# Kernel optimization log

Hardware: AMD Instinct MI355X
Metric: run time of the kernel (lower is better)

Reference implementation:

```python
import jax, jax.numpy as jnp
import numpy as np

BETA = 0.9
THRESHOLD = 1.0

B, T, I, H, O = 64, 512, 256, 512, 256


def setup_inputs() -> dict:
    key = jax.random.key(0)
    ks = jax.random.split(key, 10)
    s_in = 1.0 / np.sqrt(I)
    s_h = 1.0 / np.sqrt(H)
    return {
        "x": jax.random.normal(ks[0], (B, T, I), dtype=jnp.float32),
        "W_in": jax.random.uniform(ks[1], (H, I), jnp.float32, -s_in, s_in),
        "b_in": jax.random.uniform(ks[2], (H,), jnp.float32, -s_in, s_in),
        "W_ih": jax.random.uniform(ks[3], (H, H), jnp.float32, -s_h, s_h),
        "b_ih": jax.random.uniform(ks[4], (H,), jnp.float32, -s_h, s_h),
        "W_hh": jax.random.uniform(ks[5], (H, H), jnp.float32, -s_h, s_h),
        "b_hh": jax.random.uniform(ks[6], (H,), jnp.float32, -s_h, s_h),
        "W_out": jax.random.uniform(ks[7], (O, H), jnp.float32, -s_h, s_h),
        "b_out": jax.random.uniform(ks[8], (O,), jnp.float32, -s_h, s_h),
        "temporal_attention": jax.random.normal(ks[9], (T, O), dtype=jnp.float32),
    }


def _lif(mem, cur):
    # LIF with 'subtract' reset: new_mem*(1-s) + s*(new_mem-thr) == new_mem - s*thr
    new_mem = BETA * mem + cur
    spike = (new_mem > THRESHOLD).astype(new_mem.dtype)
    return new_mem - spike * THRESHOLD, spike


def reference(x, W_in, b_in, W_ih, b_ih, W_hh, b_hh, W_out, b_out, temporal_attention):
    dtype = x.dtype
    batch, time_steps, _ = x.shape
    hidden = W_in.shape[0]

    # Input projection for all time steps at once: (B,T,H) -> scan over T.
    input_proj = jnp.einsum('bti,hi->tbh', x, W_in) + b_in  # (T,B,H)

    mem0 = jnp.zeros((batch, hidden), dtype=dtype)
    _, hidden_spikes = jax.lax.scan(_lif, mem0, input_proj)  # (T,B,H)

    # Recurrent layer: input->hidden projection precomputed; hidden->hidden uses
    # carried membrane potential (as in the torch module).
    in_proj = jnp.einsum('tbh,gh->tbg', hidden_spikes, W_ih) + b_ih  # (T,B,H)

    def rec_step(mem, ip):
        total = ip + mem @ W_hh.T + b_hh
        return _lif(mem, total)

    _, temporal_spikes = jax.lax.scan(rec_step, mem0, in_proj)  # (T,B,H)

    out_proj = jnp.einsum('tbh,oh->tbo', temporal_spikes, W_out) + b_out  # (T,B,O)

    attn = jax.nn.softmax(temporal_attention[:time_steps], axis=0)  # (T,O)
    attended = jnp.einsum('tbo,to->bo', out_proj, attn)  # (B,O)

    # Final LIF from zero membrane: new_mem = attended; spike = (attended > thr)
    final_spikes = (attended > THRESHOLD).astype(dtype)
    return final_spikes
```

## Files before the change

### kernel.cpp

```cpp
#include <hip/hip_runtime.h>
#include <hip/hip_bf16.h>
#include <cstdint>


#define T_STEPS 512
#define BATCH 64
#define HID 512
#define IN_DIM 256
#define OUT_DIM 256
#define BETA 0.9f
#define THR 1.0f
#define SENT 0x7FC00000u

typedef __attribute__((ext_vector_type(8))) short short8;
typedef __attribute__((ext_vector_type(4))) float float4v;
typedef unsigned short ushort_t;

__global__ __launch_bounds__(256) void k_fill_nan(uint32_t* __restrict__ P) {
  const int idx = blockIdx.x * 256 + threadIdx.x;
  uint4 s = make_uint4(SENT, SENT, SENT, SENT);
  uint4* p4 = (uint4*)P;
  for (int i = idx; i < (32768 * 512) / 4; i += 65536) p4[i] = s;
}

__global__ __launch_bounds__(256) void k_split(const float* __restrict__ src,
                                               ushort_t* __restrict__ hi,
                                               ushort_t* __restrict__ lo, int n) {
  int i = blockIdx.x * 256 + threadIdx.x;
  const int stride = gridDim.x * 256;
  for (; i < n; i += stride) {
    float v = src[i];
    uint32_t u = __float_as_uint(v);
    uint32_t rh = u + 0x7FFFu + ((u >> 16) & 1u);
    ushort_t h = (ushort_t)(rh >> 16);
    float hf = __uint_as_float(((uint32_t)h) << 16);
    float l = v - hf;
    uint32_t ul = __float_as_uint(l);
    uint32_t rl = ul + 0x7FFFu + ((ul >> 16) & 1u);
    hi[i] = h;
    lo[i] = (ushort_t)(rl >> 16);
  }
}

__global__ __launch_bounds__(256) void k_softmax_t(
    const float* __restrict__ TA, float* __restrict__ attn) {
  __shared__ float redm[8][32];
  __shared__ float reds[8][32];
  const int ol = threadIdx.x & 31;
  const int tg = threadIdx.x >> 5;
  const int o = blockIdx.x * 32 + ol;
  float mx = -1e30f;
  for (int i = 0; i < 64; ++i) {
    float v = TA[(size_t)(tg * 64 + i) * OUT_DIM + o];
    mx = fmaxf(mx, v);
  }
  redm[tg][ol] = mx;
  __syncthreads();
  float m = redm[0][ol];
#pragma unroll
  for (int j = 1; j < 8; ++j) m = fmaxf(m, redm[j][ol]);
  float s = 0.f;
  for (int i = 0; i < 64; ++i) {
    float v = TA[(size_t)(tg * 64 + i) * OUT_DIM + o];
    s += __expf(v - m);
  }
  reds[tg][ol] = s;
  __syncthreads();
  float tot = 0.f;
#pragma unroll
  for (int j = 0; j < 8; ++j) tot += reds[j][ol];
  const float inv = 1.0f / tot;
  for (int i = 0; i < 64; ++i) {
    int t = tg * 64 + i;
    float v = TA[(size_t)t * OUT_DIM + o];
    attn[(size_t)t * OUT_DIM + o] = __expf(v - m) * inv;
  }
}

__global__ __launch_bounds__(256) void k_gemm_split3(
    const ushort_t* __restrict__ Ahi, const ushort_t* __restrict__ Alo,
    const ushort_t* __restrict__ Bhi, const ushort_t* __restrict__ Blo,
    const float* __restrict__ bias, float* __restrict__ C,
    int M, int N, int K) {
  __shared__ ushort_t At[2][128 * 40];
  __shared__ ushort_t Bt[2][128 * 40];
  const int tid = threadIdx.x;
  const int row0 = blockIdx.x * 128, col0 = blockIdx.y * 128;
  const int w = tid >> 6, lane = tid & 63;
  const int wm = (w >> 1) * 64, wn = (w & 1) * 64;
  const int l15 = lane & 15, quad = lane >> 4;
  float4v acc[4][4];
#pragma unroll
  for (int i = 0; i < 4; ++i)
#pragma unroll
    for (int j = 0; j < 4; ++j) acc[i][j] = (float4v){0.f, 0.f, 0.f, 0.f};

  for (int k0 = 0; k0 < K; k0 += 32) {
#pragma unroll
    for (int it = 0; it < 2; ++it) {
      int idx = it * 256 + tid;
      int r = idx >> 2;
      int c8 = (idx & 3) << 3;
      *(uint4*)(&At[0][r * 40 + c8]) =
          *(const uint4*)(&Ahi[(size_t)(row0 + r) * K + k0 + c8]);
      *(uint4*)(&At[1][r * 40 + c8]) =
          *(const uint4*)(&Alo[(size_t)(row0 + r) * K + k0 + c8]);
      *(uint4*)(&Bt[0][r * 40 + c8]) =
          *(const uint4*)(&Bhi[(size_t)(col0 + r) * K + k0 + c8]);
      *(uint4*)(&Bt[1][r * 40 + c8]) =
          *(const uint4*)(&Blo[(size_t)(col0 + r) * K + k0 + c8]);
    }
    __syncthreads();
    short8 ah[4], al[4], bh[4], bl[4];
    const int koff = quad * 8;
#pragma unroll
    for (int i = 0; i < 4; ++i) {
      ah[i] = *(const short8*)(&At[0][(wm + i * 16 + l15) * 40 + koff]);
      al[i] = *(const short8*)(&At[1][(wm + i * 16 + l15) * 40 + koff]);
      bh[i] = *(const short8*)(&Bt[0][(wn + i * 16 + l15) * 40 + koff]);
      bl[i] = *(const short8*)(&Bt[1][(wn + i * 16 + l15) * 40 + koff]);
    }
#pragma unroll
    for (int i = 0; i < 4; ++i)
#pragma unroll
      for (int j = 0; j < 4; ++j) {
        acc[i][j] = __builtin_amdgcn_mfma_f32_16x16x32_bf16(ah[i], bh[j], acc[i][j], 0, 0, 0);
        acc[i][j] = __builtin_amdgcn_mfma_f32_16x16x32_bf16(ah[i], bl[j], acc[i][j], 0, 0, 0);
        acc[i][j] = __builtin_amdgcn_mfma_f32_16x16x32_bf16(al[i], bh[j], acc[i][j], 0, 0, 0);
      }
    __syncthreads();
  }
#pragma unroll
  for (int j = 0; j < 4; ++j) {
    const int col = col0 + wn + j * 16 + l15;
    const float bv = bias ? bias[col] : 0.f;
#pragma unroll
    for (int i = 0; i < 4; ++i) {
#pragma unroll
      for (int r = 0; r < 4; ++r) {
        int row = row0 + wm + i * 16 + quad * 4 + r;
        C[(size_t)row * N + col] = acc[i][j][r] + bv;
      }
    }
  }
}

__global__ __launch_bounds__(256) void k_gemm_spike2(
    const float* __restrict__ A, const ushort_t* __restrict__ Bhi,
    const ushort_t* __restrict__ Blo, const float* __restrict__ bias,
    float* __restrict__ C, int M, int N, int K) {
  __shared__ ushort_t At[128 * 72];
  __shared__ ushort_t Bt[2][128 * 72];
  const int tid = threadIdx.x;
  const int row0 = blockIdx.x * 128, col0 = blockIdx.y * 128;
  const int w = tid >> 6, lane = tid & 63;
  const int wm = (w >> 1) * 64, wn = (w & 1) * 64;
  const int l15 = lane & 15, quad = lane >> 4;
  float4v acc[4][4];
#pragma unroll
  for (int i = 0; i < 4; ++i)
#pragma unroll
    for (int j = 0; j < 4; ++j) acc[i][j] = (float4v){0.f, 0.f, 0.f, 0.f};

  for (int k0 = 0; k0 < K; k0 += 64) {
#pragma unroll
    for (int it = 0; it < 4; ++it) {
      int idx = it * 256 + tid;
      int r = idx >> 3;
      int c8 = (idx & 7) << 3;
      uint4 pa = *(const uint4*)(&A[(size_t)(row0 + r) * K + k0 + c8]);
      uint4 pb = *(const uint4*)(&A[(size_t)(row0 + r) * K + k0 + c8 + 4]);
      uint4 st;
      st.x = (pa.x >> 16) | (pa.y & 0xFFFF0000u);
      st.y = (pa.z >> 16) | (pa.w & 0xFFFF0000u);
      st.z = (pb.x >> 16) | (pb.y & 0xFFFF0000u);
      st.w = (pb.z >> 16) | (pb.w & 0xFFFF0000u);
      *(uint4*)(&At[r * 72 + c8]) = st;
      *(uint4*)(&Bt[0][r * 72 + c8]) =
          *(const uint4*)(&Bhi[(size_t)(col0 + r) * K + k0 + c8]);
      *(uint4*)(&Bt[1][r * 72 + c8]) =
          *(const uint4*)(&Blo[(size_t)(col0 + r) * K + k0 + c8]);
    }
    __syncthreads();
#pragma unroll
    for (int ks = 0; ks < 2; ++ks) {
      short8 a[4], bh[4], bl[4];
      const int koff = ks * 32 + quad * 8;
#pragma unroll
      for (int i = 0; i < 4; ++i) {
        a[i] = *(const short8*)(&At[(wm + i * 16 + l15) * 72 + koff]);
        bh[i] = *(const short8*)(&Bt[0][(wn + i * 16 + l15) * 72 + koff]);
        bl[i] = *(const short8*)(&Bt[1][(wn + i * 16 + l15) * 72 + koff]);
      }
#pragma unroll
      for (int i = 0; i < 4; ++i)
#pragma unroll
        for (int j = 0; j < 4; ++j) {
          acc[i][j] = __builtin_amdgcn_mfma_f32_16x16x32_bf16(a[i], bh[j], acc[i][j], 0, 0, 0);
          acc[i][j] = __builtin_amdgcn_mfma_f32_16x16x32_bf16(a[i], bl[j], acc[i][j], 0, 0, 0);
        }
    }
    __syncthreads();
  }
#pragma unroll
  for (int j = 0; j < 4; ++j) {
    const int col = col0 + wn + j * 16 + l15;
    const float bv = bias ? bias[col] : 0.f;
#pragma unroll
    for (int i = 0; i < 4; ++i) {
#pragma unroll
      for (int r = 0; r < 4; ++r) {
        int row = row0 + wm + i * 16 + quad * 4 + r;
        C[(size_t)row * N + col] = acc[i][j][r] + bv;
      }
    }
  }
}

__global__ __launch_bounds__(256) void k_lif1(float* __restrict__ p) {
  const int id = blockIdx.x * 256 + threadIdx.x;
  const size_t base = (size_t)(id >> 9) * (T_STEPS * HID) + (id & 511);
  float mem = 0.f;
  for (int t0 = 0; t0 < T_STEPS; t0 += 8) {
    float v[8];
#pragma unroll
    for (int j = 0; j < 8; ++j) v[j] = p[base + (size_t)(t0 + j) * HID];
#pragma unroll
    for (int j = 0; j < 8; ++j) {
      float nm = BETA * mem + v[j];
      float sp = nm > THR ? 1.0f : 0.0f;
      p[base + (size_t)(t0 + j) * HID] = sp;
      mem = nm - sp;
    }
  }
}

__global__ __launch_bounds__(512) void k_recurrent_cp(
    const float* __restrict__ W, const float* __restrict__ b_hh,
    float* __restrict__ rp, float* __restrict__ P) {
  const int tid = threadIdx.x;
  const int grp = blockIdx.x >> 3;
  const int j = blockIdx.x & 7;
  const int seg = tid >> 6;
  const int gl = tid & 63;
  const int g0 = j << 6;

  __shared__ float memLDS[2][HID];
  __shared__ float scratch[8][2][64];

  for (int i = tid; i < 2 * HID; i += 512) ((float*)memLDS)[i] = 0.f;

  float Wreg[64];
  {
    const float* wrow = W + (size_t)(g0 + gl) * HID + (seg << 6);
#pragma unroll
    for (int k4 = 0; k4 < 16; ++k4) {
      float4 w4 = *(const float4*)(wrow + 4 * k4);
      Wreg[4 * k4 + 0] = w4.x; Wreg[4 * k4 + 1] = w4.y;
      Wreg[4 * k4 + 2] = w4.z; Wreg[4 * k4 + 3] = w4.w;
    }
  }

  const int ob = tid >> 6;
  const int ogl = tid & 63;
  const int og = g0 + ogl;
  const size_t rp_base = (size_t)(grp * 2 + ob) * (T_STEPS * HID) + og;
  float bhh_v = 0.f;
  if (tid < 128) bhh_v = b_hh[og];

  const int rg = (tid < g0) ? tid : tid + 64;

  const uint32_t* Pu = (const uint32_t*)P;
  float* Pf = P;

  __syncthreads();

  for (int t = 0; t < T_STEPS; ++t) {
    float ip_v = 0.f;
    if (tid < 128) ip_v = rp[rp_base + (size_t)t * HID];

    if (t > 0 && tid < 448) {
      const size_t slot = ((size_t)(t - 1) * 32 + grp) * 1024;
      uint32_t u0 = __hip_atomic_load(Pu + slot + rg, __ATOMIC_RELAXED,
                                      __HIP_MEMORY_SCOPE_AGENT);
      uint32_t u1 = __hip_atomic_load(Pu + slot + 512 + rg, __ATOMIC_RELAXED,
                                      __HIP_MEMORY_SCOPE_AGENT);
      while (u0 == SENT || u1 == SENT) {
        __builtin_amdgcn_s_sleep(1);
        if (u0 == SENT)
          u0 = __hip_atomic_load(Pu + slot + rg, __ATOMIC_RELAXED,
                                 __HIP_MEMORY_SCOPE_AGENT);
        if (u1 == SENT)
          u1 = __hip_atomic_load(Pu + slot + 512 + rg, __ATOMIC_RELAXED,
                                 __HIP_MEMORY_SCOPE_AGENT);
      }
      memLDS[0][rg] = __uint_as_float(u0);
      memLDS[1][rg] = __uint_as_float(u1);
    }
    __syncthreads();

    float p0a = 0.f, p0b = 0.f, p1a = 0.f, p1b = 0.f;
    {
      const float4* m0 = (const float4*)&memLDS[0][seg << 6];
      const float4* m1 = (const float4*)&memLDS[1][seg << 6];
#pragma unroll
      for (int k4 = 0; k4 < 16; ++k4) {
        float4 a = m0[k4];
        float4 b = m1[k4];
        p0a = fmaf(Wreg[4 * k4 + 0], a.x, p0a);
        p0b = fmaf(Wreg[4 * k4 + 1], a.y, p0b);
        p0a = fmaf(Wreg[4 * k4 + 2], a.z, p0a);
        p0b = fmaf(Wreg[4 * k4 + 3], a.w, p0b);
        p1a = fmaf(Wreg[4 * k4 + 0], b.x, p1a);
        p1b = fmaf(Wreg[4 * k4 + 1], b.y, p1b);
        p1a = fmaf(Wreg[4 * k4 + 2], b.z, p1a);
        p1b = fmaf(Wreg[4 * k4 + 3], b.w, p1b);
      }
    }
    scratch[seg][0][gl] = p0a + p0b;
    scratch[seg][1][gl] = p1a + p1b;
    __syncthreads();

    if (tid < 128) {
      float s = 0.f;
#pragma unroll
      for (int ss = 0; ss < 8; ++ss) s += scratch[ss][ob][ogl];
      const float m_old = memLDS[ob][og];
      const float nm = BETA * m_old + ip_v + s + bhh_v;
      const float sp = nm > THR ? 1.0f : 0.0f;
      rp[rp_base + (size_t)t * HID] = sp;
      const float mnew = nm - sp;
      memLDS[ob][og] = mnew;
      const size_t slot = ((size_t)t * 32 + grp) * 1024;
      __hip_atomic_store(Pf + slot + (size_t)ob * 512 + og, mnew,
                         __ATOMIC_RELAXED, __HIP_MEMORY_SCOPE_AGENT);
    }
  }
}

__global__ __launch_bounds__(256) void k_attend(
    const float* __restrict__ op, const float* __restrict__ attn,
    const float* __restrict__ b_out, float* __restrict__ out) {
  const int b = blockIdx.x;
  const int o = threadIdx.x;
  float s = b_out[o];
  const float* opb = op + (size_t)b * T_STEPS * OUT_DIM + o;
  for (int t0 = 0; t0 < T_STEPS; t0 += 8) {
    float av[8], pv[8];
#pragma unroll
    for (int j = 0; j < 8; ++j) {
      av[j] = attn[(size_t)(t0 + j) * OUT_DIM + o];
      pv[j] = opb[(size_t)(t0 + j) * OUT_DIM];
    }
#pragma unroll
    for (int j = 0; j < 8; ++j) s = fmaf(av[j], pv[j], s);
  }
  out[b * OUT_DIM + o] = s > THR ? 1.0f : 0.0f;
}

extern "C" void kernel_launch(void* const* d_in, const int* in_sizes, int n_in,
                              void* d_out, int out_size, void* d_ws, size_t ws_size,
                              hipStream_t stream) {
  (void)in_sizes; (void)n_in; (void)out_size; (void)ws_size;
  const float* x     = (const float*)d_in[0];
  const float* W_in  = (const float*)d_in[1];
  const float* b_in  = (const float*)d_in[2];
  const float* W_ih  = (const float*)d_in[3];
  const float* b_ih  = (const float*)d_in[4];
  const float* W_hh  = (const float*)d_in[5];
  const float* b_hh  = (const float*)d_in[6];
  const float* W_out = (const float*)d_in[7];
  const float* b_out = (const float*)d_in[8];
  const float* TA    = (const float*)d_in[9];

  float* ws = (float*)d_ws;
  float* proj  = ws;
  float* rproj = proj + (size_t)32768 * 512;
  float* attn  = rproj + (size_t)32768 * 512;
  ushort_t* wih_hi = (ushort_t*)(attn + 512 * 256);
  ushort_t* wih_lo = wih_hi + 512 * 512;
  ushort_t* win_hi = wih_lo + 512 * 512;
  ushort_t* win_lo = win_hi + 512 * 256;
  ushort_t* wout_hi = win_lo + 512 * 256;
  ushort_t* wout_lo = wout_hi + 256 * 512;
  ushort_t* x_hi = (ushort_t*)rproj;
  ushort_t* x_lo = x_hi + (size_t)32768 * 256;
  float* P = proj;
  float* out_proj = proj;

  k_softmax_t<<<8, 256, 0, stream>>>(TA, attn);
  k_split<<<4096, 256, 0, stream>>>(x, x_hi, x_lo, 32768 * 256);
  k_split<<<512, 256, 0, stream>>>(W_in, win_hi, win_lo, 512 * 256);
  k_split<<<512, 256, 0, stream>>>(W_ih, wih_hi, wih_lo, 512 * 512);
  k_split<<<512, 256, 0, stream>>>(W_out, wout_hi, wout_lo, 256 * 512);

  k_gemm_split3<<<dim3(256, 4), 256, 0, stream>>>(
      x_hi, x_lo, win_hi, win_lo, b_in, proj, 32768, 512, 256);
  k_lif1<<<128, 256, 0, stream>>>(proj);
  k_gemm_spike2<<<dim3(256, 4), 256, 0, stream>>>(
      proj, wih_hi, wih_lo, b_ih, rproj, 32768, 512, 512);
  k_fill_nan<<<256, 256, 0, stream>>>((uint32_t*)P);
  k_recurrent_cp<<<256, 512, 0, stream>>>(W_hh, b_hh, rproj, P);
  k_gemm_spike2<<<dim3(256, 2), 256, 0, stream>>>(
      rproj, wout_hi, wout_lo, nullptr, out_proj, 32768, 256, 512);
  k_attend<<<64, 256, 0, stream>>>(out_proj, attn, b_out, (float*)d_out);
}
```

Before: 1.077 ms.

## Restructure recurrent step: in-wave swizzle reduction, double-buffered LDS, tighter spin polling

Remaps the recurrent kernel's work so each wave covers 8 output rows with 8 lanes per row. The cross-segment reduction now uses ds_swizzle inside the wave instead of an LDS scratch array, which removes one __syncthreads per timestep. Membrane state is kept in registers and the LDS buffer is double-buffered by step parity and padded to 72 floats per row to reduce bank conflicts. Spin polling now re-issues loads without sleeping for the first tries, which cuts wakeup latency but adds memory traffic.

```diff
diff --git a/kernel.cpp b/kernel.cpp
--- a/kernel.cpp
+++ b/kernel.cpp
@@ -239,20 +239,22 @@
     const float* __restrict__ W, const float* __restrict__ b_hh,
     float* __restrict__ rp, float* __restrict__ P) {
   const int tid = threadIdx.x;
-  const int grp = blockIdx.x >> 3;
-  const int j = blockIdx.x & 7;
-  const int seg = tid >> 6;
-  const int gl = tid & 63;
-  const int g0 = j << 6;
-
-  __shared__ float memLDS[2][HID];
-  __shared__ float scratch[8][2][64];
-
-  for (int i = tid; i < 2 * HID; i += 512) ((float*)memLDS)[i] = 0.f;
+  const int grp = blockIdx.x & 31;
+  const int j   = blockIdx.x >> 5;
+  const int w   = tid >> 6;
+  const int l   = tid & 63;
+  const int q   = l >> 3;
+  const int c   = l & 7;
+  const int row = (w << 3) + q;
+  const int g0  = j << 6;
+
+  __shared__ float memLDS[2][2][8 * 72];
+
+  for (int i = tid; i < 2 * 2 * 8 * 72; i += 512) ((float*)memLDS)[i] = 0.f;
 
   float Wreg[64];
   {
-    const float* wrow = W + (size_t)(g0 + gl) * HID + (seg << 6);
+    const float* wrow = W + (size_t)(g0 + row) * HID + (c << 6);
 #pragma unroll
     for (int k4 = 0; k4 < 16; ++k4) {
       float4 w4 = *(const float4*)(wrow + 4 * k4);
@@ -261,14 +263,15 @@
     }
   }
 
-  const int ob = tid >> 6;
-  const int ogl = tid & 63;
-  const int og = g0 + ogl;
-  const size_t rp_base = (size_t)(grp * 2 + ob) * (T_STEPS * HID) + og;
-  float bhh_v = 0.f;
-  if (tid < 128) bhh_v = b_hh[og];
+  const bool lif = (c == 0);
+  const int og = g0 + row;
+  const size_t rp_b0 = (size_t)(grp * 2 + 0) * (T_STEPS * HID) + og;
+  const size_t rp_b1 = (size_t)(grp * 2 + 1) * (T_STEPS * HID) + og;
+  const float bhh_v = lif ? b_hh[og] : 0.f;
+  float mem0 = 0.f, mem1 = 0.f;
 
   const int rg = (tid < g0) ? tid : tid + 64;
+  const int raddr = (rg >> 6) * 72 + (rg & 63);
 
   const uint32_t* Pu = (const uint32_t*)P;
   float* Pf = P;
@@ -276,33 +279,40 @@
   __syncthreads();
 
   for (int t = 0; t < T_STEPS; ++t) {
-    float ip_v = 0.f;
-    if (tid < 128) ip_v = rp[rp_base + (size_t)t * HID];
-
+    const int par = t & 1;
+    float ip0 = 0.f, ip1 = 0.f;
+    if (lif) {
+      ip0 = rp[rp_b0 + (size_t)t * HID];
+      ip1 = rp[rp_b1 + (size_t)t * HID];
+    }
     if (t > 0 && tid < 448) {
       const size_t slot = ((size_t)(t - 1) * 32 + grp) * 1024;
-      uint32_t u0 = __hip_atomic_load(Pu + slot + rg, __ATOMIC_RELAXED,
-                                      __HIP_MEMORY_SCOPE_AGENT);
-      uint32_t u1 = __hip_atomic_load(Pu + slot + 512 + rg, __ATOMIC_RELAXED,
-                                      __HIP_MEMORY_SCOPE_AGENT);
-      while (u0 == SENT || u1 == SENT) {
-        __builtin_amdgcn_s_sleep(1);
-        if (u0 == SENT)
-          u0 = __hip_atomic_load(Pu + slot + rg, __ATOMIC_RELAXED,
-                                 __HIP_MEMORY_SCOPE_AGENT);
-        if (u1 == SENT)
-          u1 = __hip_atomic_load(Pu + slot + 512 + rg, __ATOMIC_RELAXED,
-                                 __HIP_MEMORY_SCOPE_AGENT);
-      }
-      memLDS[0][rg] = __uint_as_float(u0);
-      memLDS[1][rg] = __uint_as_float(u1);
+      const uint32_t* a0p = Pu + slot + rg;
+      const uint32_t* a1p = a0p + 512;
+      uint32_t u0 = __hip_atomic_load(a0p, __ATOMIC_RELAXED, __HIP_MEMORY_SCOPE_AGENT);
+      uint32_t u1 = __hip_atomic_load(a1p, __ATOMIC_RELAXED, __HIP_MEMORY_SCOPE_AGENT);
+      if (u0 == SENT || u1 == SENT) {
+        uint32_t v0 = __hip_atomic_load(a0p, __ATOMIC_RELAXED, __HIP_MEMORY_SCOPE_AGENT);
+        uint32_t v1 = __hip_atomic_load(a1p, __ATOMIC_RELAXED, __HIP_MEMORY_SCOPE_AGENT);
+        int tries = 0;
+        do {
+          uint32_t w0 = __hip_atomic_load(a0p, __ATOMIC_RELAXED, __HIP_MEMORY_SCOPE_AGENT);
+          uint32_t w1 = __hip_atomic_load(a1p, __ATOMIC_RELAXED, __HIP_MEMORY_SCOPE_AGENT);
+          if (u0 == SENT) u0 = v0;
+          if (u1 == SENT) u1 = v1;
+          v0 = w0; v1 = w1;
+          if (++tries > 24) __builtin_amdgcn_s_sleep(1);
+        } while (u0 == SENT || u1 == SENT);
+      }
+      memLDS[par][0][raddr] = __uint_as_float(u0);
+      memLDS[par][1][raddr] = __uint_as_float(u1);
     }
     __syncthreads();
 
     float p0a = 0.f, p0b = 0.f, p1a = 0.f, p1b = 0.f;
     {
-      const float4* m0 = (const float4*)&memLDS[0][seg << 6];
-      const float4* m1 = (const float4*)&memLDS[1][seg << 6];
+      const float4* m0 = (const float4*)&memLDS[par][0][c * 72];
+      const float4* m1 = (const float4*)&memLDS[par][1][c * 72];
 #pragma unroll
       for (int k4 = 0; k4 < 16; ++k4) {
         float4 a = m0[k4];
@@ -317,23 +327,30 @@
         p1b = fmaf(Wreg[4 * k4 + 3], b.w, p1b);
       }
     }
-    scratch[seg][0][gl] = p0a + p0b;
-    scratch[seg][1][gl] = p1a + p1b;
-    __syncthreads();
-
-    if (tid < 128) {
-      float s = 0.f;
-#pragma unroll
-      for (int ss = 0; ss < 8; ++ss) s += scratch[ss][ob][ogl];
-      const float m_old = memLDS[ob][og];
-      const float nm = BETA * m_old + ip_v + s + bhh_v;
-      const float sp = nm > THR ? 1.0f : 0.0f;
-      rp[rp_base + (size_t)t * HID] = sp;
-      const float mnew = nm - sp;
-      memLDS[ob][og] = mnew;
+    const int i0 = __float_as_int(p0a + p0b);
+    const int i1 = __float_as_int(p1a + p1b);
+    float s0 = 0.f, s1 = 0.f;
+#define RED(ss)                                                                 \
+    s0 += __int_as_float(__builtin_amdgcn_ds_swizzle(i0, ((ss) << 5) | 0x18)); \
+    s1 += __int_as_float(__builtin_amdgcn_ds_swizzle(i1, ((ss) << 5) | 0x18));
+    RED(0) RED(1) RED(2) RED(3) RED(4) RED(5) RED(6) RED(7)
+#undef RED
+
+    if (lif) {
+      const int npar = par ^ 1;
       const size_t slot = ((size_t)t * 32 + grp) * 1024;
-      __hip_atomic_store(Pf + slot + (size_t)ob * 512 + og, mnew,
-                         __ATOMIC_RELAXED, __HIP_MEMORY_SCOPE_AGENT);
+      const float nm0 = BETA * mem0 + ip0 + s0 + bhh_v;
+      const float sp0 = nm0 > THR ? 1.0f : 0.0f;
+      mem0 = nm0 - sp0;
+      __hip_atomic_store(Pf + slot + og, mem0, __ATOMIC_RELAXED, __HIP_MEMORY_SCOPE_AGENT);
+      const float nm1 = BETA * mem1 + ip1 + s1 + bhh_v;
+      const float sp1 = nm1 > THR ? 1.0f : 0.0f;
+      mem1 = nm1 - sp1;
+      __hip_atomic_store(Pf + slot + 512 + og, mem1, __ATOMIC_RELAXED, __HIP_MEMORY_SCOPE_AGENT);
+      rp[rp_b0 + (size_t)t * HID] = sp0;
+      rp[rp_b1 + (size_t)t * HID] = sp1;
+      memLDS[npar][0][j * 72 + row] = mem0;
+      memLDS[npar][1][j * 72 + row] = mem1;
     }
   }
 }
```

Result: faster. 1.049 ms (-2.6%).
